# Optimization experiments

Hardware: AMD Instinct MI355X
Metric: run time of the kernel (lower is better)

## Reference

```python
import jax, jax.numpy as jnp
import numpy as np

B = 32768   # batch
F = 32      # per-node feature dim
H = 256     # hidden width
M = 4       # modules per node
OUT = 8     # final output dim
INIT_W = 0.003
B_INIT = 0.1


def _lin(k, din, dout):
    # fanin_init-style uniform weights, bias filled with 0.1 (hidden layers)
    s = 1.0 / np.sqrt(din)
    W = jax.random.uniform(k, (M, din, dout), jnp.float32, -s, s)
    b = jnp.full((M, dout), B_INIT, jnp.float32)
    return W, b


def setup_inputs() -> dict:
    key = jax.random.key(0)
    ks = jax.random.split(key, 16)
    feats = jax.random.normal(ks[0], (B, 4 * F), jnp.float32)
    idx = jax.random.randint(ks[1], (B, 4), 0, M)
    onehots = jax.nn.one_hot(idx, M, dtype=jnp.float32).reshape(B, 4 * M)
    input_val = jnp.concatenate([feats, onehots], axis=1)  # [B,144]

    W00, b00 = _lin(ks[2], F, H)        # node0 post layer 0
    W01, b01 = _lin(ks[3], H, H)        # node0 post layer 1
    Wpre1, bpre1 = _lin(ks[4], F, H)    # node1 pre
    Wpost1, bpost1 = _lin(ks[5], 2 * H, H)  # node1 interface (prev 256 + own 256)
    Wpre2, bpre2 = _lin(ks[6], F, H)
    Wpost2, bpost2 = _lin(ks[7], 2 * H, H)
    Wpre3, bpre3 = _lin(ks[8], F, H)
    Wpost3, bpost3 = _lin(ks[9], 2 * H, H)
    # final output layer: uniform(-init_w, init_w) for W and b, identity act
    Wfin3 = jax.random.uniform(ks[10], (M, H, OUT), jnp.float32, -INIT_W, INIT_W)
    bfin3 = jax.random.uniform(ks[11], (M, OUT), jnp.float32, -INIT_W, INIT_W)
    return dict(input_val=input_val,
                W00=W00, b00=b00, W01=W01, b01=b01,
                Wpre1=Wpre1, bpre1=bpre1, Wpost1=Wpost1, bpost1=bpost1,
                Wpre2=Wpre2, bpre2=bpre2, Wpost2=Wpost2, bpost2=bpost2,
                Wpre3=Wpre3, bpre3=bpre3, Wpost3=Wpost3, bpost3=bpost3,
                Wfin3=Wfin3, bfin3=bfin3)


def _select(h, onehot):
    # per-row pick of the assigned module's output: [B,M,D],[B,M] -> [B,D]
    return jnp.einsum('bmo,bm->bo', h, onehot)


def reference(input_val, W00, b00, W01, b01,
              Wpre1, bpre1, Wpost1, bpost1,
              Wpre2, bpre2, Wpost2, bpost2,
              Wpre3, bpre3, Wpost3, bpost3,
              Wfin3, bfin3):
    feat = lambda j: input_val[:, j * F:(j + 1) * F]
    oh = lambda j: input_val[:, 4 * F + j * M: 4 * F + (j + 1) * M]

    # node 0: two hidden layers, module-dispatched (dense-all-modules + one-hot combine)
    h = jax.nn.relu(jnp.einsum('bi,mio->bmo', feat(0), W00) + b00)
    h = jax.nn.relu(jnp.einsum('bmi,mio->bmo', h, W01) + b01)
    x = _select(h, oh(0))  # [B,H]

    def node(x_prev, fj, ohj, Wpre, bpre, Wpost, bpost):
        hp = jax.nn.relu(jnp.einsum('bi,mio->bmo', fj, Wpre) + bpre)
        # interface layer consumes concat([x_prev, hp]); split the weight to
        # avoid materializing [B,M,2H]
        hq = jax.nn.relu(jnp.einsum('bi,mio->bmo', x_prev, Wpost[:, :H, :])
                         + jnp.einsum('bmi,mio->bmo', hp, Wpost[:, H:, :])
                         + bpost)
        return hq  # [B,M,H]

    x = _select(node(x, feat(1), oh(1), Wpre1, bpre1, Wpost1, bpost1), oh(1))
    x = _select(node(x, feat(2), oh(2), Wpre2, bpre2, Wpost2, bpost2), oh(2))

    h3 = node(x, feat(3), oh(3), Wpre3, bpre3, Wpost3, bpost3)  # [B,M,H]
    out = jnp.einsum('bmi,mio->bmo', h3, Wfin3) + bfin3          # final linear, identity act
    return _select(out, oh(3))  # [B,OUT]
```

## Files before the change

### kernel.cpp

```cpp
#include <hip/hip_runtime.h>

#define NB 32768
#define MAXTILE 1280
#define ROWS 32
#define NT 2

typedef short s8v __attribute__((ext_vector_type(8)));
typedef short s4v __attribute__((ext_vector_type(4)));
typedef float f4v __attribute__((ext_vector_type(4)));
typedef unsigned short u16;
typedef unsigned short u16x4 __attribute__((ext_vector_type(4)));
typedef unsigned int u32;
typedef unsigned char u8;

__device__ __forceinline__ float bf2f(u16 u) { return __uint_as_float(((u32)u) << 16); }
__device__ __forceinline__ u16 f2bf(float f) {
    u32 x = __float_as_uint(f);
    x += 0x7FFFu + ((x >> 16) & 1u);
    return (u16)(x >> 16);
}
__device__ __forceinline__ s8v ld8(const u16* p) { return *reinterpret_cast<const s8v*>(p); }

#define MFMA16(a, b, c) __builtin_amdgcn_mfma_f32_16x16x32_bf16((a), (b), (c), 0, 0, 0)

__device__ __forceinline__ void detect_flag(const void* input, int tid, int* shflag)
{
    if (tid < 64) {
        u32 w = ((const u32*)input)[tid];
        u32 h0 = w & 0xFFFFu;
        u32 e0 = (h0 >> 7) & 0xFFu;
        bool plaus = (h0 == 0u) || (e0 >= 96u && e0 <= 143u);
        unsigned long long m = __ballot(plaus);
        if (tid == 0) *shflag = (__popcll(m) >= 48) ? 1 : 0;
    }
}

struct RepArgs {
    const void* W01; const void* Wp[3]; const void* pre[4]; const void* fin;
    const void* bias[9];
    u16 *rPre, *rW01, *rWp[3], *rFin, *cbias;
};

__global__ __launch_bounds__(256) void prepA_kernel(const void* __restrict__ inputv,
                                                    int* __restrict__ gcnt,
                                                    int* __restrict__ perm2,
                                                    u16* __restrict__ feats16,
                                                    RepArgs R)
{
    __shared__ int lcnt[256];
    __shared__ int sBase[256];
    __shared__ u16 T[8192];
    __shared__ int shmisc;
    int tid = threadIdx.x;
    int b = blockIdx.x;
    detect_flag(inputv, tid, &shmisc);
    __syncthreads();
    int flag = shmisc;

    if (b < 128) {
        lcnt[tid] = 0;
        __syncthreads();
        int row = (b << 8) + tid;
        const u32* in32 = (const u32*)inputv;
        const u16* in16 = (const u16*)inputv;
        int key = 0;
        if (flag) {
#pragma unroll
            for (int j = 0; j < 4; j++) {
                u16x4 v = *(const u16x4*)(in16 + row * 144 + 128 + j * 4);
                int m = v[1] ? 1 : (v[2] ? 2 : (v[3] ? 3 : 0));
                key |= m << (j << 1);
            }
        } else {
#pragma unroll
            for (int j = 0; j < 4; j++) {
                const u32* p = in32 + row * 144 + 128 + j * 4;
                u32 v1 = p[1], v2 = p[2], v3 = p[3];
                int m = v1 ? 1 : (v2 ? 2 : (v3 ? 3 : 0));
                key |= m << (j << 1);
            }
        }
        int loc = atomicAdd(&lcnt[key], 1);
        __syncthreads();
        int c = lcnt[tid];
        sBase[tid] = c ? atomicAdd(&gcnt[tid], c) : 0;
        __syncthreads();
        int slot = sBase[key] + loc;
        if (slot < 512) perm2[(key << 9) + slot] = row;

        int r0 = b << 8;
        if (flag) {
            for (int i = tid; i < 256 * 16; i += 256) {
                int r = r0 + (i >> 4), j = (i & 15) << 3;
                *(s8v*)(feats16 + ((size_t)r << 7) + j) = ld8(in16 + (size_t)r * 144 + j);
            }
        } else {
            for (int i = tid; i < 256 * 32; i += 256) {
                int r = r0 + (i >> 5), j = (i & 31) << 2;
                f4v f = *(const f4v*)(in32 + (size_t)r * 144 + j);
                s4v p;
#pragma unroll
                for (int q = 0; q < 4; q++) p[q] = (short)f2bf(f[q]);
                *(s4v*)(feats16 + ((size_t)r << 7) + j) = p;
            }
        }
        return;
    }

    int rb = b - 128;
    const void* src = nullptr; u16* dst = nullptr; int K = 0, k0 = 0, mrow = 0;
    if (rb < 32) {
        int m = rb >> 3, s = rb & 7;
        src = R.W01; dst = R.rW01 + (m * 8 + s) * 8192; K = 256; k0 = s * 32; mrow = m;
    } else if (rb < 224) {
        int idx = rb - 32, mat = idx >> 6, r = idx & 63, m = r >> 4, s = r & 15;
        src = R.Wp[mat]; dst = R.rWp[mat] + (m * 16 + s) * 8192; K = 512; k0 = s * 32; mrow = m;
    } else if (rb < 240) {
        int idx = rb - 224, mat = idx >> 2, m = idx & 3;
        src = R.pre[mat]; dst = R.rPre + (mat * 4 + m) * 8192; K = 32; k0 = 0; mrow = m;
    } else if (rb < 244) {
        int m = rb - 240;
        const u16* s16 = (const u16*)R.fin;
        const float* s32 = (const float*)R.fin;
        for (int i = tid; i < 2048; i += 256) {
            int si = (m * 256 + (i >> 3)) * 8 + (i & 7);
            T[i] = flag ? s16[si] : f2bf(s32[si]);
        }
        __syncthreads();
        u16* d = R.rFin + m * 4096;
        for (int i = tid; i < 4096; i += 256) {
            int s = i >> 9, lane = (i >> 3) & 63, j = i & 7;
            int q = lane >> 4, l16 = lane & 15;
            int k = s * 32 + q * 8 + j;
            d[i] = (l16 < 8) ? T[k * 8 + l16] : (u16)0;
        }
        return;
    } else {
        const int sz[9] = {1024,1024,1024,1024,1024,1024,1024,1024,32};
        const int of[9] = {0,1024,2048,3072,4096,5120,6144,7168,8192};
        for (int i = tid; i < 8224; i += 256) {
            int t = i, e = 0;
            while (t >= sz[e]) { t -= sz[e]; e++; }
            R.cbias[of[e] + t] = flag ? ((const u16*)R.bias[e])[t]
                                      : f2bf(((const float*)R.bias[e])[t]);
        }
        return;
    }
    const u16* s16 = (const u16*)src;
    const float* s32 = (const float*)src;
    for (int i = tid; i < 8192; i += 256) {
        int k = i >> 8, n = i & 255;
        int srcIdx = (mrow * K + k0 + k) * 256 + n;
        T[i] = flag ? s16[srcIdx] : f2bf(s32[srcIdx]);
    }
    __syncthreads();
    for (int i = tid; i < 8192; i += 256) {
        int mt = i >> 9, lane = (i >> 3) & 63, j = i & 7;
        int k = ((lane >> 4) << 3) + j, n = (mt << 4) + (lane & 15);
        dst[i] = T[(k << 8) + n];
    }
}

struct MainP { const u16 *rPre, *rW01, *rWp1, *rWp2, *rWp3, *rFin, *cbias, *feats; };

__global__ __launch_bounds__(256, 5) void main_kernel(
    const void* __restrict__ inRaw,
    const int* __restrict__ gcnt, const int* __restrict__ perm2,
    MainP P, void* __restrict__ outp)
{
    __shared__ __align__(16) u16 xhB[8192];
    __shared__ int rowids[ROWS];
    __shared__ int shflag;
    __shared__ int sMeta[4];

    int tid = threadIdx.x;
    int lane = tid & 63, w = tid >> 6, quad = lane >> 4, l16 = lane & 15;

    int b = blockIdx.x;
    int t = ((b & 7) * (MAXTILE / 8)) + (b >> 3);

    detect_flag(inRaw, tid, &shflag);

    if (tid < 64) {
        int4 g = *(const int4*)(gcnt + tid * 4);
        int tot4[4] = {g.x, g.y, g.z, g.w};
        int tiles4[4], lsum = 0;
#pragma unroll
        for (int j = 0; j < 4; j++) { tiles4[j] = (tot4[j] + 31) >> 5; lsum += tiles4[j]; }
        int pre = lsum;
#pragma unroll
        for (int off = 1; off < 64; off <<= 1) {
            int v = __shfl_up(pre, off, 64);
            if (tid >= off) pre += v;
        }
        int run = pre - lsum;
#pragma unroll
        for (int j = 0; j < 4; j++) {
            if (t >= run && t < run + tiles4[j]) {
                sMeta[0] = tid * 4 + j;
                sMeta[1] = t - run;
                sMeta[2] = tot4[j];
            }
            run += tiles4[j];
        }
        if (tid == 63) sMeta[3] = pre;
    }
    __syncthreads();
    if (t >= sMeta[3]) return;
    int key = sMeta[0], tau = sMeta[1], tot = sMeta[2];
    int cntIn = tot - tau * ROWS; if (cntIn > ROWS) cntIn = ROWS;
    if (tid < ROWS) {
        int g = tid < cntIn ? tid : cntIn - 1;
        rowids[tid] = perm2[(key << 9) + tau * ROWS + g];
    }
    __syncthreads();

    int flag = shflag;
    int rows_[NT];
#pragma unroll
    for (int nt = 0; nt < NT; nt++) rows_[nt] = rowids[nt * 16 + l16];

    const u16* feats = P.feats;
    int stA = ((quad >> 1) * 16 + l16) * 8 + (quad & 1) * 4;

    f4v acc[4][NT];

    auto gemm_run = [&](const u16* Ab) {
        const u16* base = Ab + (w * 4) * 512 + lane * 8;
        s8v A[2][4];
#pragma unroll
        for (int ci = 0; ci < 4; ci++) {
            A[0][ci] = ld8(base + ci * 512);
            A[1][ci] = ld8(base + 8192 + ci * 512);
        }
        __builtin_amdgcn_s_setprio(1);
#pragma unroll
        for (int s = 0; s < 8; s++) {
            s8v B0 = ld8(&xhB[((0 * 8 + s) << 9) + lane * 8]);
            s8v B1 = ld8(&xhB[((1 * 8 + s) << 9) + lane * 8]);
            s8v c0 = A[s & 1][0], c1 = A[s & 1][1], c2 = A[s & 1][2], c3 = A[s & 1][3];
            if (s + 2 < 8) {
#pragma unroll
                for (int ci = 0; ci < 4; ci++)
                    A[s & 1][ci] = ld8(base + (s + 2) * 8192 + ci * 512);
            }
            acc[0][0] = MFMA16(c0, B0, acc[0][0]);
            acc[0][1] = MFMA16(c0, B1, acc[0][1]);
            acc[1][0] = MFMA16(c1, B0, acc[1][0]);
            acc[1][1] = MFMA16(c1, B1, acc[1][1]);
            acc[2][0] = MFMA16(c2, B0, acc[2][0]);
            acc[2][1] = MFMA16(c2, B1, acc[2][1]);
            acc[3][0] = MFMA16(c3, B0, acc[3][0]);
            acc[3][1] = MFMA16(c3, B1, acc[3][1]);
        }
        __builtin_amdgcn_s_setprio(0);
    };

    for (int node = 0; node < 4; node++) {
        int m = (key >> (node << 1)) & 3;

#pragma unroll
        for (int ci = 0; ci < 4; ci++) {
            u16x4 bv = *(const u16x4*)(P.cbias + node * 2048 + 1024 + m * 256 + (w * 4 + ci) * 16 + quad * 4);
            f4v f;
#pragma unroll
            for (int r = 0; r < 4; r++) f[r] = bf2f(bv[r]);
            acc[ci][0] = f; acc[ci][1] = f;
        }

        const u16* wb2;
        if (node > 0) {
            const u16* WB = (node == 1 ? P.rWp1 : (node == 2 ? P.rWp2 : P.rWp3)) + m * 16 * 8192;
            gemm_run(WB);
            __syncthreads();
            wb2 = WB + 8 * 8192;
        } else {
            wb2 = P.rW01 + m * 8 * 8192;
        }

        {
            s8v fb0 = ld8(feats + ((size_t)rows_[0] << 7) + (node << 5) + (quad << 3));
            s8v fb1 = ld8(feats + ((size_t)rows_[1] << 7) + (node << 5) + (quad << 3));
            const u16* preB = P.rPre + ((node << 2) + m) * 8192 + (w * 4) * 512 + lane * 8;
#pragma unroll
            for (int ci = 0; ci < 4; ci++) {
                s8v a = ld8(preB + ci * 512);
                u16x4 bv = *(const u16x4*)(P.cbias + node * 2048 + m * 256 + (w * 4 + ci) * 16 + quad * 4);
                f4v bias;
#pragma unroll
                for (int r = 0; r < 4; r++) bias[r] = bf2f(bv[r]);
                int sb = 2 * w + (ci >> 1), sub = (ci & 1) << 8;
#pragma unroll
                for (int nt = 0; nt < NT; nt++) {
                    f4v c = MFMA16(a, nt ? fb1 : fb0, bias);
                    s4v p;
#pragma unroll
                    for (int r = 0; r < 4; r++) { float v = c[r] > 0.f ? c[r] : 0.f; p[r] = (short)f2bf(v); }
                    *(s4v*)&xhB[((nt * 8 + sb) << 9) + sub + stA] = p;
                }
            }
        }
        __syncthreads();

        gemm_run(wb2);
        __syncthreads();

#pragma unroll
        for (int ci = 0; ci < 4; ci++) {
            int sb = 2 * w + (ci >> 1), sub = (ci & 1) << 8;
#pragma unroll
            for (int nt = 0; nt < NT; nt++) {
                f4v a = acc[ci][nt];
                s4v p;
#pragma unroll
                for (int r = 0; r < 4; r++) { float v = a[r] > 0.f ? a[r] : 0.f; p[r] = (short)f2bf(v); }
                *(s4v*)&xhB[((nt * 8 + sb) << 9) + sub + stA] = p;
            }
        }
        __syncthreads();
    }

    if (w < NT) {
        int m3 = (key >> 6) & 3;
        f4v c;
#pragma unroll
        for (int r = 0; r < 4; r++)
            c[r] = (quad < 2) ? bf2f(P.cbias[8192 + m3 * 8 + quad * 4 + r]) : 0.f;
#pragma unroll
        for (int s = 0; s < 8; s++) {
            s8v A = ld8(P.rFin + m3 * 4096 + s * 512 + lane * 8);
            s8v B = ld8(&xhB[((w * 8 + s) << 9) + lane * 8]);
            c = MFMA16(A, B, c);
        }
        int bidx = w * 16 + l16;
        if (quad < 2 && bidx < cntIn) {
            int row = rowids[bidx];
            if (flag) {
                s4v p;
#pragma unroll
                for (int r = 0; r < 4; r++) p[r] = (short)f2bf(c[r]);
                *(s4v*)((u16*)outp + row * 8 + quad * 4) = p;
            } else {
                *(f4v*)((float*)outp + row * 8 + quad * 4) = c;
            }
        }
    }
}

extern "C" void kernel_launch(void* const* d_in, const int* in_sizes, int n_in,
                              void* d_out, int out_size, void* d_ws, size_t ws_size,
                              hipStream_t stream)
{
    (void)in_sizes; (void)n_in; (void)out_size;
    const void* input  = d_in[0];
    const void* W00    = d_in[1];
    const void* b00    = d_in[2];
    const void* W01    = d_in[3];
    const void* b01    = d_in[4];
    const void* Wpre1  = d_in[5];
    const void* bpre1  = d_in[6];
    const void* Wpost1 = d_in[7];
    const void* bpost1 = d_in[8];
    const void* Wpre2  = d_in[9];
    const void* bpre2  = d_in[10];
    const void* Wpost2 = d_in[11];
    const void* bpost2 = d_in[12];
    const void* Wpre3  = d_in[13];
    const void* bpre3  = d_in[14];
    const void* Wpost3 = d_in[15];
    const void* bpost3 = d_in[16];
    const void* Wfin   = d_in[17];
    const void* bfin   = d_in[18];

    char* base = (char*)d_ws;
    size_t off = 0;
    auto alloc = [&](size_t bytes) -> char* {
        char* p = base + off;
        off += (bytes + 255) & ~(size_t)255;
        return p;
    };
    int*  gcnt      = (int*)alloc(256 * 4);
    int*  perm2     = (int*)alloc(256 * 512 * 4);
    u16*  feats16   = (u16*)alloc((size_t)NB * 128 * 2);
    u16*  cbias    = (u16*)alloc(8224 * 2);
    u16*  rPre     = (u16*)alloc(131072 * 2);
    u16*  rW01     = (u16*)alloc(262144 * 2);
    u16*  rWp1     = (u16*)alloc(524288 * 2);
    u16*  rWp2     = (u16*)alloc(524288 * 2);
    u16*  rWp3     = (u16*)alloc(524288 * 2);
    u16*  rFin     = (u16*)alloc(16384 * 2);
    if (off > ws_size) return;

    RepArgs R;
    R.W01 = W01; R.Wp[0] = Wpost1; R.Wp[1] = Wpost2; R.Wp[2] = Wpost3;
    R.pre[0] = W00; R.pre[1] = Wpre1; R.pre[2] = Wpre2; R.pre[3] = Wpre3;
    R.fin = Wfin;
    R.bias[0] = b00;   R.bias[1] = b01;
    R.bias[2] = bpre1; R.bias[3] = bpost1;
    R.bias[4] = bpre2; R.bias[5] = bpost2;
    R.bias[6] = bpre3; R.bias[7] = bpost3;
    R.bias[8] = bfin;
    R.rPre = rPre; R.rW01 = rW01;
    R.rWp[0] = rWp1; R.rWp[1] = rWp2; R.rWp[2] = rWp3;
    R.rFin = rFin; R.cbias = cbias;

    hipMemsetAsync(gcnt, 0, 256 * 4, stream);
    prepA_kernel<<<373, 256, 0, stream>>>(input, gcnt, perm2, feats16, R);

    MainP P;
    P.rPre = rPre; P.rW01 = rW01; P.rWp1 = rWp1; P.rWp2 = rWp2; P.rWp3 = rWp3;
    P.rFin = rFin; P.cbias = cbias; P.feats = feats16;
    main_kernel<<<MAXTILE, 256, 0, stream>>>(input, gcnt, perm2, P, d_out);
}
```

Measured before the change: 196.2 us.

## Stream weight tiles via global_load_lds into per-wave LDS ring buffer

Weight fragments now go straight from global memory into a 3-slot per-wave LDS ring using global_load_lds, with explicit vmcnt waits, instead of a register double buffer. The aim is a deeper prefetch that hides global latency and frees VGPRs. It adds 48KB of LDS per block and lowers launch bounds from 5 to 2 blocks per CU, which cuts occupancy and the ability to hide latency across waves. The hand-written waitcnt counts are fragile, and the LDS reads issued after them are not fenced against the async writes.

```diff
diff --git a/kernel.cpp b/kernel.cpp
--- a/kernel.cpp
+++ b/kernel.cpp
@@ -20,6 +20,12 @@
     return (u16)(x >> 16);
 }
 __device__ __forceinline__ s8v ld8(const u16* p) { return *reinterpret_cast<const s8v*>(p); }
+
+typedef __attribute__((address_space(1))) const unsigned int GU32;
+typedef __attribute__((address_space(3))) unsigned int LU32;
+__device__ __forceinline__ void gll16(const u16* g, u16* l) {
+    __builtin_amdgcn_global_load_lds((GU32*)g, (LU32*)l, 16, 0, 0);
+}
 
 #define MFMA16(a, b, c) __builtin_amdgcn_mfma_f32_16x16x32_bf16((a), (b), (c), 0, 0, 0)
 
@@ -163,12 +169,13 @@
 
 struct MainP { const u16 *rPre, *rW01, *rWp1, *rWp2, *rWp3, *rFin, *cbias, *feats; };
 
-__global__ __launch_bounds__(256, 5) void main_kernel(
+__global__ __launch_bounds__(256, 2) void main_kernel(
     const void* __restrict__ inRaw,
     const int* __restrict__ gcnt, const int* __restrict__ perm2,
     MainP P, void* __restrict__ outp)
 {
     __shared__ __align__(16) u16 xhB[8192];
+    __shared__ __align__(16) u16 ring[24576];
     __shared__ int rowids[ROWS];
     __shared__ int shflag;
     __shared__ int sMeta[4];
@@ -222,28 +229,38 @@
 
     const u16* feats = P.feats;
     int stA = ((quad >> 1) * 16 + l16) * 8 + (quad & 1) * 4;
+    u16* rb = &ring[w * 3 * 2048];
 
     f4v acc[4][NT];
 
     auto gemm_run = [&](const u16* Ab) {
-        const u16* base = Ab + (w * 4) * 512 + lane * 8;
-        s8v A[2][4];
-#pragma unroll
-        for (int ci = 0; ci < 4; ci++) {
-            A[0][ci] = ld8(base + ci * 512);
-            A[1][ci] = ld8(base + 8192 + ci * 512);
-        }
+        const u16* src = Ab + (w * 4) * 512 + lane * 8;
+        __builtin_amdgcn_sched_barrier(0);
+#pragma unroll
+        for (int d = 0; d < 2; d++)
+#pragma unroll
+            for (int ci = 0; ci < 4; ci++)
+                gll16(src + d * 8192 + ci * 512, rb + (d * 2048) + ci * 512);
         __builtin_amdgcn_s_setprio(1);
 #pragma unroll
         for (int s = 0; s < 8; s++) {
+            if (s + 2 < 8) {
+                __builtin_amdgcn_sched_barrier(0);
+#pragma unroll
+                for (int ci = 0; ci < 4; ci++)
+                    gll16(src + (s + 2) * 8192 + ci * 512,
+                          rb + (((s + 2) % 3) * 2048) + ci * 512);
+            }
+            if (s < 6)       asm volatile("s_waitcnt vmcnt(8)" ::: "memory");
+            else if (s == 6) asm volatile("s_waitcnt vmcnt(4)" ::: "memory");
+            else             asm volatile("s_waitcnt vmcnt(0)" ::: "memory");
+            const u16* slot = rb + (s % 3) * 2048 + lane * 8;
             s8v B0 = ld8(&xhB[((0 * 8 + s) << 9) + lane * 8]);
             s8v B1 = ld8(&xhB[((1 * 8 + s) << 9) + lane * 8]);
-            s8v c0 = A[s & 1][0], c1 = A[s & 1][1], c2 = A[s & 1][2], c3 = A[s & 1][3];
-            if (s + 2 < 8) {
-#pragma unroll
-                for (int ci = 0; ci < 4; ci++)
-                    A[s & 1][ci] = ld8(base + (s + 2) * 8192 + ci * 512);
-            }
+            s8v c0 = ld8(slot);
+            s8v c1 = ld8(slot + 512);
+            s8v c2 = ld8(slot + 1024);
+            s8v c3 = ld8(slot + 1536);
             acc[0][0] = MFMA16(c0, B0, acc[0][0]);
             acc[0][1] = MFMA16(c0, B1, acc[0][1]);
             acc[1][0] = MFMA16(c1, B0, acc[1][0]);
@@ -254,6 +271,7 @@
             acc[3][1] = MFMA16(c3, B1, acc[3][1]);
         }
         __builtin_amdgcn_s_setprio(0);
+        __builtin_amdgcn_sched_barrier(0);
     };
 
     for (int node = 0; node < 4; node++) {
```

New measurement: 210.9 us. 1.08x slower.

## Stream weight tiles through LDS with async global_load_lds triple buffering

Applied to the files above, without the earlier changes.

Replaces the per-wave register double-buffered global loads of weight fragments with a three-slot LDS ring filled by direct global-to-LDS loads, using vmcnt waits and a block barrier each k-step. The aim is to cut VGPR pressure and hide global latency. The cost is 48 KB of extra shared memory, an occupancy hint lowered from 5 to 2, and a block-wide barrier on every one of the 8 steps. The loss of occupancy and the added barriers may outweigh the latency hiding.

```diff
diff --git a/kernel.cpp b/kernel.cpp
--- a/kernel.cpp
+++ b/kernel.cpp
@@ -20,6 +20,12 @@
     return (u16)(x >> 16);
 }
 __device__ __forceinline__ s8v ld8(const u16* p) { return *reinterpret_cast<const s8v*>(p); }
+
+typedef __attribute__((address_space(1))) const unsigned int GU32;
+typedef __attribute__((address_space(3))) unsigned int LU32;
+__device__ __forceinline__ void gll16(const u16* g, u16* l) {
+    __builtin_amdgcn_global_load_lds((GU32*)g, (LU32*)l, 16, 0, 0);
+}
 
 #define MFMA16(a, b, c) __builtin_amdgcn_mfma_f32_16x16x32_bf16((a), (b), (c), 0, 0, 0)
 
@@ -163,12 +169,13 @@
 
 struct MainP { const u16 *rPre, *rW01, *rWp1, *rWp2, *rWp3, *rFin, *cbias, *feats; };
 
-__global__ __launch_bounds__(256, 5) void main_kernel(
+__global__ __launch_bounds__(256, 2) void main_kernel(
     const void* __restrict__ inRaw,
     const int* __restrict__ gcnt, const int* __restrict__ perm2,
     MainP P, void* __restrict__ outp)
 {
     __shared__ __align__(16) u16 xhB[8192];
+    __shared__ __align__(16) u16 bufs[24576];
     __shared__ int rowids[ROWS];
     __shared__ int shflag;
     __shared__ int sMeta[4];
@@ -226,24 +233,31 @@
     f4v acc[4][NT];
 
     auto gemm_run = [&](const u16* Ab) {
-        const u16* base = Ab + (w * 4) * 512 + lane * 8;
-        s8v A[2][4];
-#pragma unroll
-        for (int ci = 0; ci < 4; ci++) {
-            A[0][ci] = ld8(base + ci * 512);
-            A[1][ci] = ld8(base + 8192 + ci * 512);
-        }
+        auto stage = [&](int d, int slot) {
+            __builtin_amdgcn_sched_barrier(0);
+#pragma unroll
+            for (int c = 0; c < 4; c++)
+                gll16(Ab + d * 8192 + c * 2048 + w * 512 + lane * 8,
+                      bufs + slot * 8192 + c * 2048 + w * 512);
+            __builtin_amdgcn_sched_barrier(0);
+        };
+        stage(0, 0);
+        stage(1, 1);
         __builtin_amdgcn_s_setprio(1);
 #pragma unroll
         for (int s = 0; s < 8; s++) {
+            if (s < 7) asm volatile("s_waitcnt vmcnt(4)" ::: "memory");
+            else       asm volatile("s_waitcnt vmcnt(0)" ::: "memory");
+            __builtin_amdgcn_s_barrier();
+            __builtin_amdgcn_sched_barrier(0);
+            if (s + 2 < 8) stage(s + 2, (s + 2) % 3);
+            const u16* buf = bufs + (s % 3) * 8192 + (w * 4) * 512 + lane * 8;
             s8v B0 = ld8(&xhB[((0 * 8 + s) << 9) + lane * 8]);
             s8v B1 = ld8(&xhB[((1 * 8 + s) << 9) + lane * 8]);
-            s8v c0 = A[s & 1][0], c1 = A[s & 1][1], c2 = A[s & 1][2], c3 = A[s & 1][3];
-            if (s + 2 < 8) {
-#pragma unroll
-                for (int ci = 0; ci < 4; ci++)
-                    A[s & 1][ci] = ld8(base + (s + 2) * 8192 + ci * 512);
-            }
+            s8v c0 = ld8(buf);
+            s8v c1 = ld8(buf + 512);
+            s8v c2 = ld8(buf + 1024);
+            s8v c3 = ld8(buf + 1536);
             acc[0][0] = MFMA16(c0, B0, acc[0][0]);
             acc[0][1] = MFMA16(c0, B1, acc[0][1]);
             acc[1][0] = MFMA16(c1, B0, acc[1][0]);
@@ -254,6 +268,7 @@
             acc[3][1] = MFMA16(c3, B1, acc[3][1]);
         }
         __builtin_amdgcn_s_setprio(0);
+        __builtin_amdgcn_sched_barrier(0);
     };
 
     for (int node = 0; node < 4; node++) {
```

Result: slower. 230.8 us (+17.7%).
